# Optimization experiments

Hardware: AMD Instinct MI355X
Metric: run time of the kernel (lower is better)

Reference implementation:

```python
import jax, jax.numpy as jnp
import numpy as np

B, T, D_MODEL, N_HEADS = 2, 2048, 1024, 16
HEAD_DIM = D_MODEL // N_HEADS
EPS = 1e-6
ROPE_BASE = 10000.0


def _rope_cos_sin(seq_len, dim, offset=0, dtype=jnp.float32):
    half = dim // 2
    inv_freq = 1.0 / (ROPE_BASE ** (jnp.arange(half, dtype=jnp.float32) / half))
    pos = jnp.arange(offset, offset + seq_len, dtype=jnp.float32)
    freqs = pos[:, None] * inv_freq[None, :]              # (T, half)
    emb = jnp.concatenate([freqs, freqs], axis=-1)        # (T, dim)
    return jnp.cos(emb).astype(dtype), jnp.sin(emb).astype(dtype)


def _rotate_half(x):
    x1, x2 = jnp.split(x, 2, axis=-1)
    return jnp.concatenate([-x2, x1], axis=-1)


def setup_inputs() -> dict:
    key = jax.random.key(0)
    k1, k2, k3 = jax.random.split(key, 3)
    x = jax.random.normal(k1, (B, T, D_MODEL), dtype=jnp.float32)
    norm_w = jnp.ones((D_MODEL,), dtype=jnp.float32)
    w_qkv = jax.random.normal(k2, (3 * D_MODEL, D_MODEL), dtype=jnp.float32) * 0.02
    w_out = jax.random.normal(k3, (D_MODEL, D_MODEL), dtype=jnp.float32) * 0.02
    return {"x": x, "norm_w": norm_w, "w_qkv": w_qkv, "w_out": w_out}


def reference(x, norm_w, w_qkv, w_out):
    # RMSNorm (pre-norm)
    h = x * jax.lax.rsqrt(jnp.mean(jnp.square(x), axis=-1, keepdims=True) + EPS) * norm_w
    # Fused QKV projection: (B,T,3*D)
    qkv = jnp.einsum('btd,ed->bte', h, w_qkv).reshape(B, T, 3, N_HEADS, HEAD_DIM)
    q, k, v = qkv[:, :, 0], qkv[:, :, 1], qkv[:, :, 2]   # each (B,T,H,Dh)
    # RoPE on q, k (offset=0)
    cos, sin = _rope_cos_sin(T, HEAD_DIM, dtype=q.dtype)
    cos = cos[None, :, None, :]
    sin = sin[None, :, None, :]
    q = q * cos + _rotate_half(q) * sin
    k = k * cos + _rotate_half(k) * sin
    # Causal scaled dot-product attention
    scale = 1.0 / np.sqrt(HEAD_DIM)
    scores = jnp.einsum('bqhd,bkhd->bhqk', q, k) * scale  # (B,H,T,T)
    causal = jnp.tril(jnp.ones((T, T), dtype=bool))
    scores = jnp.where(causal[None, None], scores, jnp.finfo(scores.dtype).min)
    attn = jax.nn.softmax(scores, axis=-1)
    out = jnp.einsum('bhqk,bkhd->bqhd', attn, v).reshape(B, T, D_MODEL)
    out = jnp.einsum('btd,ed->bte', out, w_out)
    return x + out
```

## Files before the change

### kernel.cpp

```cpp
#include <hip/hip_runtime.h>
#include <math.h>

typedef unsigned short u16;
typedef unsigned int u32;
typedef __attribute__((ext_vector_type(4))) float f32x4;
typedef __attribute__((ext_vector_type(8))) short s16x8;

#define GLL16(g, l) __builtin_amdgcn_global_load_lds( \
    (const __attribute__((address_space(1))) void*)(g), \
    (__attribute__((address_space(3))) void*)(l), 16, 0, 0)

#define MFMA16(a, b, c) __builtin_amdgcn_mfma_f32_16x16x32_bf16(a, b, c, 0, 0, 0)

__device__ __forceinline__ u16 f2bf(float f) {
  union { float f; u32 u; } v; v.f = f;
  u32 r = v.u + 0x7FFFu + ((v.u >> 16) & 1u);
  return (u16)(r >> 16);
}
__device__ __forceinline__ float bf2f(u16 h) {
  union { u32 u; float f; } v; v.u = ((u32)h) << 16;
  return v.f;
}
__device__ __forceinline__ u32 pk2bf(float lo, float hi) {
  union { float f; u32 u; } a, b; a.f = lo; b.f = hi;
  return __builtin_amdgcn_perm(b.u + 0x8000u, a.u + 0x8000u, 0x07060302u);
}
__device__ __forceinline__ float fexp2(float x) {
#if __has_builtin(__builtin_amdgcn_exp2f)
  return __builtin_amdgcn_exp2f(x);
#else
  return exp2f(x);
#endif
}

__global__ __launch_bounds__(256) void prep_kernel(const float* __restrict__ x,
                                                   const float* __restrict__ wgt,
                                                   const float* __restrict__ w_qkv,
                                                   const float* __restrict__ w_out,
                                                   u16* __restrict__ h,
                                                   u16* __restrict__ wqkv_b,
                                                   u16* __restrict__ wout_b) {
  __shared__ float red[4];
  const int bid = blockIdx.x, tid = threadIdx.x;
  if (bid < 4096) {
    const int row = bid;
    const float4 v = *(const float4*)&x[(size_t)row * 1024 + tid * 4];
    float ss = v.x * v.x + v.y * v.y + v.z * v.z + v.w * v.w;
    ss += __shfl_xor(ss, 1);  ss += __shfl_xor(ss, 2);  ss += __shfl_xor(ss, 4);
    ss += __shfl_xor(ss, 8);  ss += __shfl_xor(ss, 16); ss += __shfl_xor(ss, 32);
    if ((tid & 63) == 0) red[tid >> 6] = ss;
    __syncthreads();
    const float tot = red[0] + red[1] + red[2] + red[3];
    const float s = rsqrtf(tot * (1.0f / 1024.0f) + 1e-6f);
    const float4 g = *(const float4*)&wgt[tid * 4];
    uint2 o;
    o.x = (u32)f2bf(v.x * s * g.x) | ((u32)f2bf(v.y * s * g.y) << 16);
    o.y = (u32)f2bf(v.z * s * g.z) | ((u32)f2bf(v.w * s * g.w) << 16);
    *(uint2*)&h[(size_t)row * 1024 + tid * 4] = o;
  } else if (bid < 7168) {
    int i = (bid - 4096) * 256 + tid;
    float4 v = ((const float4*)w_qkv)[i];
    uint2 o;
    o.x = (u32)f2bf(v.x) | ((u32)f2bf(v.y) << 16);
    o.y = (u32)f2bf(v.z) | ((u32)f2bf(v.w) << 16);
    ((uint2*)wqkv_b)[i] = o;
  } else {
    int i = (bid - 7168) * 256 + tid;
    float4 v = ((const float4*)w_out)[i];
    uint2 o;
    o.x = (u32)f2bf(v.x) | ((u32)f2bf(v.y) << 16);
    o.y = (u32)f2bf(v.z) | ((u32)f2bf(v.w) << 16);
    ((uint2*)wout_b)[i] = o;
  }
}

template <int EPI>
__global__ __launch_bounds__(256) void gemm_bt(const u16* __restrict__ A,
                                               const u16* __restrict__ Bt,
                                               u16* __restrict__ Cb,
                                               float* __restrict__ Cf,
                                               const float* __restrict__ resid,
                                               int M, int N, int K) {
  __shared__ __attribute__((aligned(16))) u16 As[128 * 32];
  __shared__ __attribute__((aligned(16))) u16 Bs[128 * 32];
  const int tid = threadIdx.x;
  const int w = tid >> 6, lane = tid & 63;
  const int quad = lane >> 4, l16 = lane & 15;
  const int gm0 = blockIdx.y * 128, gn0 = blockIdx.x * 128;
  const int wm = (w & 1) * 64, wn = (w >> 1) * 64;

  f32x4 acc[4][4] = {};

  for (int k0 = 0; k0 < K; k0 += 32) {
    __syncthreads();
    if (w < 2) {
      #pragma unroll
      for (int i = 0; i < 4; ++i) {
        int sb = (w * 4 + i) * 64;
        int slot = sb + lane;
        int m = slot >> 2, c = (slot & 3) ^ (m & 3);
        GLL16(A + (size_t)(gm0 + m) * K + k0 + c * 8, &As[sb * 8]);
      }
    } else {
      #pragma unroll
      for (int i = 0; i < 4; ++i) {
        int sb = ((w - 2) * 4 + i) * 64;
        int slot = sb + lane;
        int n = slot >> 2, c = (slot & 3) ^ (n & 3);
        GLL16(Bt + (size_t)(gn0 + n) * K + k0 + c * 8, &Bs[sb * 8]);
      }
    }
    __syncthreads();
    s16x8 aF[4], bF[4];
    #pragma unroll
    for (int i = 0; i < 4; ++i) {
      int m = wm + i * 16 + l16;
      aF[i] = *(const s16x8*)&As[(m * 4 + (quad ^ (m & 3))) * 8];
    }
    #pragma unroll
    for (int j = 0; j < 4; ++j) {
      int n = wn + j * 16 + l16;
      bF[j] = *(const s16x8*)&Bs[(n * 4 + (quad ^ (n & 3))) * 8];
    }
    #pragma unroll
    for (int i = 0; i < 4; ++i)
      #pragma unroll
      for (int j = 0; j < 4; ++j)
        acc[i][j] = MFMA16(aF[i], bF[j], acc[i][j]);
  }

  #pragma unroll
  for (int i = 0; i < 4; ++i) {
    int row0 = gm0 + wm + i * 16 + quad * 4;
    #pragma unroll
    for (int j = 0; j < 4; ++j) {
      int col = gn0 + wn + j * 16 + l16;
      #pragma unroll
      for (int r = 0; r < 4; ++r) {
        size_t idx = (size_t)(row0 + r) * N + col;
        if (EPI == 0) Cb[idx] = f2bf(acc[i][j][r]);
        else          Cf[idx] = acc[i][j][r] + resid[idx];
      }
    }
  }
}

__global__ __launch_bounds__(512, 2) void gemm256(const u16* __restrict__ A,
                                                  const u16* __restrict__ Bt,
                                                  u16* __restrict__ Cb) {
  __shared__ __attribute__((aligned(16))) char smem[131072];
  const int tid = threadIdx.x;
  const int w = tid >> 6, lane = tid & 63;
  const int quad = lane >> 4, l16 = lane & 15;
  const int wr = w >> 2, wc = w & 3;
  const int rsw = l16 & 7;
  const int id = blockIdx.x;
  const int sw = (id & 7) * 24 + (id >> 3);
  const int by = sw / 12, bx = sw - by * 12;
  const int gm0 = by * 256, gn0 = bx * 256;
  const int scg = (lane & 7) ^ (lane >> 3);

  auto STAGE_HALF = [&](int kt, int part) {
    const int sb = (kt & 1) * 65536 + (part >> 1) * 32768 + (part & 1) * 16384;
    const u16* src = (part >> 1) ? Bt : A;
    const int g0 = ((part >> 1) ? gn0 : gm0) + (part & 1) * 128;
    const int k0 = kt * 64;
    #pragma unroll
    for (int q = 0; q < 2; ++q) {
      int r = q * 64 + (tid >> 3);
      GLL16(src + (size_t)(g0 + r) * 1024 + k0 + scg * 8,
            smem + sb + q * 8192 + w * 1024);
    }
  };

  f32x4 acc[8][4] = {};

  #pragma unroll
  for (int n = 0; n < 8; ++n) STAGE_HALF(n >> 2, n & 3);
  __syncthreads();

  for (int kt = 0; kt < 16; ++kt) {
    const char* Ab = smem + (kt & 1) * 65536;
    const char* Bb = Ab + 32768;
    const int arow = wr * 128 + l16;
    const int brow = wc * 64 + l16;
    s16x8 aA[4][2], bB[4][2];

    #pragma unroll
    for (int fi = 0; fi < 4; ++fi) {
      const char* p = Ab + (arow + fi * 16) * 128;
      aA[fi][0] = *(const s16x8*)(p + ((quad ^ rsw) * 16));
      aA[fi][1] = *(const s16x8*)(p + (((4 + quad) ^ rsw) * 16));
    }
    #pragma unroll
    for (int fj = 0; fj < 2; ++fj) {
      const char* p = Bb + (brow + fj * 16) * 128;
      bB[fj][0] = *(const s16x8*)(p + ((quad ^ rsw) * 16));
      bB[fj][1] = *(const s16x8*)(p + (((4 + quad) ^ rsw) * 16));
    }
    if (kt >= 1 && kt < 15) STAGE_HALF(kt + 1, 0);
    __builtin_amdgcn_s_barrier();
    asm volatile("s_waitcnt lgkmcnt(0)" ::: "memory");
    __builtin_amdgcn_sched_barrier(0);
    __builtin_amdgcn_s_setprio(1);
    #pragma unroll
    for (int fi = 0; fi < 4; ++fi)
      #pragma unroll
      for (int fj = 0; fj < 2; ++fj) {
        acc[fi][fj] = MFMA16(aA[fi][0], bB[fj][0], acc[fi][fj]);
        acc[fi][fj] = MFMA16(aA[fi][1], bB[fj][1], acc[fi][fj]);
      }
    __builtin_amdgcn_s_setprio(0);
    __builtin_amdgcn_s_barrier();
    asm volatile("" ::: "memory");

    #pragma unroll
    for (int fj = 0; fj < 2; ++fj) {
      const char* p = Bb + (brow + (2 + fj) * 16) * 128;
      bB[2 + fj][0] = *(const s16x8*)(p + ((quad ^ rsw) * 16));
      bB[2 + fj][1] = *(const s16x8*)(p + (((4 + quad) ^ rsw) * 16));
    }
    if (kt >= 1 && kt < 15) STAGE_HALF(kt + 1, 1);
    __builtin_amdgcn_s_barrier();
    asm volatile("s_waitcnt lgkmcnt(0)" ::: "memory");
    __builtin_amdgcn_sched_barrier(0);
    __builtin_amdgcn_s_setprio(1);
    #pragma unroll
    for (int fi = 0; fi < 4; ++fi)
      #pragma unroll
      for (int fj = 0; fj < 2; ++fj) {
        acc[fi][2 + fj] = MFMA16(aA[fi][0], bB[2 + fj][0], acc[fi][2 + fj]);
        acc[fi][2 + fj] = MFMA16(aA[fi][1], bB[2 + fj][1], acc[fi][2 + fj]);
      }
    __builtin_amdgcn_s_setprio(0);
    __builtin_amdgcn_s_barrier();
    asm volatile("" ::: "memory");

    #pragma unroll
    for (int fi = 0; fi < 4; ++fi) {
      const char* p = Ab + (arow + (4 + fi) * 16) * 128;
      aA[fi][0] = *(const s16x8*)(p + ((quad ^ rsw) * 16));
      aA[fi][1] = *(const s16x8*)(p + (((4 + quad) ^ rsw) * 16));
    }
    if (kt < 14) STAGE_HALF(kt + 2, 2);
    __builtin_amdgcn_s_barrier();
    asm volatile("s_waitcnt lgkmcnt(0)" ::: "memory");
    __builtin_amdgcn_sched_barrier(0);
    __builtin_amdgcn_s_setprio(1);
    #pragma unroll
    for (int fi = 0; fi < 4; ++fi)
      #pragma unroll
      for (int fj = 0; fj < 2; ++fj) {
        acc[4 + fi][fj] = MFMA16(aA[fi][0], bB[fj][0], acc[4 + fi][fj]);
        acc[4 + fi][fj] = MFMA16(aA[fi][1], bB[fj][1], acc[4 + fi][fj]);
      }
    __builtin_amdgcn_s_setprio(0);
    __builtin_amdgcn_s_barrier();
    asm volatile("" ::: "memory");

    if (kt < 14) STAGE_HALF(kt + 2, 3);
    __builtin_amdgcn_s_barrier();
    __builtin_amdgcn_s_setprio(1);
    #pragma unroll
    for (int fi = 0; fi < 4; ++fi)
      #pragma unroll
      for (int fj = 0; fj < 2; ++fj) {
        acc[4 + fi][2 + fj] = MFMA16(aA[fi][0], bB[2 + fj][0], acc[4 + fi][2 + fj]);
        acc[4 + fi][2 + fj] = MFMA16(aA[fi][1], bB[2 + fj][1], acc[4 + fi][2 + fj]);
      }
    __builtin_amdgcn_s_setprio(0);
    if (kt < 14)      asm volatile("s_waitcnt vmcnt(4)" ::: "memory");
    else if (kt < 15) asm volatile("s_waitcnt vmcnt(0)" ::: "memory");
    __builtin_amdgcn_s_barrier();
    asm volatile("" ::: "memory");
  }

  #pragma unroll
  for (int g = 0; g < 8; ++g) {
    const int row0 = gm0 + wr * 128 + g * 16 + quad * 4;
    #pragma unroll
    for (int fj = 0; fj < 4; ++fj) {
      const int col = gn0 + wc * 64 + fj * 16 + l16;
      #pragma unroll
      for (int r = 0; r < 4; ++r)
        Cb[(size_t)(row0 + r) * 3072 + col] = f2bf(acc[g][fj][r]);
    }
  }
}

__global__ __launch_bounds__(256) void rope_kernel(const u16* __restrict__ qkv,
                                                   u16* __restrict__ Qr,
                                                   u16* __restrict__ Kr,
                                                   u16* __restrict__ Vt) {
  const int tt = blockIdx.x, bh = blockIdx.y;
  const int b = bh >> 4, h = bh & 15;
  const int tid = threadIdx.x;
  const float QSCALE = 0.125f * 1.4426950408889634f;

  #pragma unroll
  for (int ii = 0; ii < 8; ++ii) {
    int idx = ii * 256 + tid;
    int tl = idx >> 5, jj = idx & 31;
    int t = tt * 64 + tl;
    size_t mrow = (size_t)(b * 2048 + t) * 3072 + h * 64;
    float q1 = bf2f(qkv[mrow + jj]),        q2 = bf2f(qkv[mrow + 32 + jj]);
    float k1 = bf2f(qkv[mrow + 1024 + jj]), k2 = bf2f(qkv[mrow + 1024 + 32 + jj]);
    float invf = exp2f(-(float)jj * (13.287712379549449f / 32.0f));
    float ang = (float)t * invf;
    float sn, cs;
    sincosf(ang, &sn, &cs);
    size_t orow = (size_t)(bh * 2048 + t) * 64;
    Qr[orow + jj]      = f2bf((q1 * cs - q2 * sn) * QSCALE);
    Qr[orow + 32 + jj] = f2bf((q2 * cs + q1 * sn) * QSCALE);
    Kr[orow + jj]      = f2bf(k1 * cs - k2 * sn);
    Kr[orow + 32 + jj] = f2bf(k2 * cs + k1 * sn);
  }

  __shared__ __attribute__((aligned(16))) u16 Vl[64][72];
  for (int s = tid; s < 512; s += 256) {
    int r = s >> 3, c8 = (s & 7) * 8;
    *(uint4*)&Vl[r][c8] =
        *(const uint4*)&qkv[(size_t)(b * 2048 + tt * 64 + r) * 3072 + 2048 + h * 64 + c8];
  }
  __syncthreads();
  for (int s = tid; s < 512; s += 256) {
    int d = s >> 3, t8 = (s & 7) * 8;
    u16 tmp[8];
    #pragma unroll
    for (int k = 0; k < 8; ++k) tmp[k] = Vl[t8 + k][d];
    *(uint4*)&Vt[(size_t)(bh * 64 + d) * 2048 + tt * 64 + t8] = *(uint4*)tmp;
  }
}

__global__ __launch_bounds__(512, 2) void attn_kernel(const u16* __restrict__ Qr,
                                                      const u16* __restrict__ Kr,
                                                      const u16* __restrict__ Vt,
                                                      u16* __restrict__ AO) {
  __shared__ __attribute__((aligned(16))) char smem[102400];
  const int tid = threadIdx.x;
  const int w = tid >> 6, lane = tid & 63;
  const int wq = w & 3, wp = w >> 2;
  const int quad = lane >> 4, l16 = lane & 15;
  const int id = blockIdx.x;
  const int bh = id & 31;
  const int c  = id >> 5;
  const int b = bh >> 4, h = bh & 15;
  const size_t qkb = (size_t)bh * (2048 * 64);
  const size_t vtb = (size_t)bh * (64 * 2048);
  u16* Pw = (u16*)(smem + 65536 + w * 4608);

  const int srow = lane >> 3;
  const int scg  = (lane & 7) ^ srow;
  const int smat = w & 1, stp = (w >> 1) & 1, shalf = (w >> 2) & 1;

  auto STAGE = [&](int j0, int d) {
    const int jn = j0 + stp;
    if (smat == 0) {
      #pragma unroll
      for (int ii = 0; ii < 4; ++ii) {
        int i = shalf * 4 + ii;
        GLL16(Kr + qkb + (size_t)(jn * 64 + i * 8 + srow) * 64 + scg * 8,
              smem + (stp * 2 + d) * 8192 + i * 1024);
      }
    } else {
      #pragma unroll
      for (int ii = 0; ii < 4; ++ii) {
        int i = shalf * 4 + ii;
        GLL16(Vt + vtb + (size_t)(i * 8 + srow) * 2048 + jn * 64 + scg * 8,
              smem + 32768 + (stp * 2 + d) * 8192 + i * 1024);
      }
    }
  };

  for (int t = 0; t < 2; ++t) {
    const int qblk = t ? (15 - c) : c;
    const int q0w = qblk * 128 + wq * 32;
    const int steps = qblk + 1;

    s16x8 bQ[2][2];
    #pragma unroll
    for (int s = 0; s < 2; ++s)
      #pragma unroll
      for (int hf = 0; hf < 2; ++hf)
        bQ[s][hf] = *(const s16x8*)&Qr[qkb + (size_t)(q0w + s * 16 + l16) * 64 + hf * 32 + quad * 8];

    f32x4 O[2][4] = {};
    float l_run[2] = {0.0f, 0.0f};

    STAGE(0, 0);
    __syncthreads();

    for (int st = 0; st < steps; ++st) {
      const int cur = st & 1;
      if (st + 1 < steps) STAGE(2 * st + 2, cur ^ 1);

      const int j = 2 * st + wp;
      if (j * 64 <= q0w + 31) {
        const u16* Kb = (const u16*)(smem + (wp * 2 + cur) * 8192);
        const u16* Vb = (const u16*)(smem + 32768 + (wp * 2 + cur) * 8192);
        const bool masked = (j * 64 + 63 > q0w);
        const int rsw = (l16 & 7);

        s16x8 aK[4][2];
        #pragma unroll
        for (int kt = 0; kt < 4; ++kt)
          #pragma unroll
          for (int hf = 0; hf < 2; ++hf)
            aK[kt][hf] = *(const s16x8*)&Kb[(kt * 16 + l16) * 64 + (((hf * 4 + quad) ^ rsw) * 8)];

        f32x4 S[2][4];
        __builtin_amdgcn_s_setprio(1);
        #pragma unroll
        for (int kt = 0; kt < 4; ++kt)
          #pragma unroll
          for (int s = 0; s < 2; ++s) {
            f32x4 z = {};
            z = MFMA16(aK[kt][0], bQ[s][0], z);
            S[s][kt] = MFMA16(aK[kt][1], bQ[s][1], z);
          }
        __builtin_amdgcn_s_setprio(0);

        if (masked) {
          #pragma unroll
          for (int s = 0; s < 2; ++s) {
            int q = q0w + s * 16 + l16;
            #pragma unroll
            for (int kt = 0; kt < 4; ++kt) {
              int key0 = j * 64 + kt * 16 + quad * 4;
              #pragma unroll
              for (int r = 0; r < 4; ++r)
                if (key0 + r > q) S[s][kt][r] = -1e30f;
            }
          }
        }

        #pragma unroll
        for (int s = 0; s < 2; ++s) {
          float sum = 0.0f;
          #pragma unroll
          for (int kt = 0; kt < 4; ++kt) {
            #pragma unroll
            for (int r = 0; r < 4; ++r) {
              float e = fexp2(S[s][kt][r]);
              S[s][kt][r] = e;
              sum += e;
            }
          }
          sum += __shfl_xor(sum, 16);
          sum += __shfl_xor(sum, 32);
          l_run[s] += sum;
          #pragma unroll
          for (int kt = 0; kt < 4; ++kt) {
            uint2 pw;
            pw.x = pk2bf(S[s][kt][0], S[s][kt][1]);
            pw.y = pk2bf(S[s][kt][2], S[s][kt][3]);
            *(uint2*)&Pw[s * 1152 + l16 * 72 + kt * 16 + quad * 4] = pw;
          }
        }

        s16x8 bP[2][2];
        #pragma unroll
        for (int s = 0; s < 2; ++s) {
          bP[s][0] = *(const s16x8*)&Pw[s * 1152 + l16 * 72 + quad * 8];
          bP[s][1] = *(const s16x8*)&Pw[s * 1152 + l16 * 72 + 32 + quad * 8];
        }
        s16x8 aV[4][2];
        #pragma unroll
        for (int dt = 0; dt < 4; ++dt)
          #pragma unroll
          for (int hf = 0; hf < 2; ++hf)
            aV[dt][hf] = *(const s16x8*)&Vb[(dt * 16 + l16) * 64 + (((hf * 4 + quad) ^ rsw) * 8)];

        __builtin_amdgcn_s_setprio(1);
        #pragma unroll
        for (int dt = 0; dt < 4; ++dt)
          #pragma unroll
          for (int s = 0; s < 2; ++s) {
            O[s][dt] = MFMA16(aV[dt][0], bP[s][0], O[s][dt]);
            O[s][dt] = MFMA16(aV[dt][1], bP[s][1], O[s][dt]);
          }
        __builtin_amdgcn_s_setprio(0);
      }

      __syncthreads();
    }

    if (wp == 1) {
      float* Lsl = (float*)(smem + 65536 + wq * 512);
      Lsl[lane]      = l_run[0];
      Lsl[64 + lane] = l_run[1];
      f32x4* slot = (f32x4*)smem + wq * 512;
      #pragma unroll
      for (int s = 0; s < 2; ++s)
        #pragma unroll
        for (int dt = 0; dt < 4; ++dt)
          slot[(s * 4 + dt) * 64 + lane] = O[s][dt];
    }
    __syncthreads();
    if (wp == 0) {
      const float* Lsl = (const float*)(smem + 65536 + wq * 512);
      const f32x4* slot = (const f32x4*)smem + wq * 512;
      #pragma unroll
      for (int s = 0; s < 2; ++s) {
        float l_tot = l_run[s] + Lsl[s * 64 + lane];
        float inv = __builtin_amdgcn_rcpf(l_tot);
        int q = q0w + s * 16 + l16;
        #pragma unroll
        for (int dt = 0; dt < 4; ++dt) {
          f32x4 o = O[s][dt] + slot[(s * 4 + dt) * 64 + lane];
          uint2 ow;
          ow.x = pk2bf(o[0] * inv, o[1] * inv);
          ow.y = pk2bf(o[2] * inv, o[3] * inv);
          *(uint2*)&AO[(size_t)(b * 2048 + q) * 1024 + h * 64 + dt * 16 + quad * 4] = ow;
        }
      }
    }
    __syncthreads();
  }
}

extern "C" void kernel_launch(void* const* d_in, const int* in_sizes, int n_in,
                              void* d_out, int out_size, void* d_ws, size_t ws_size,
                              hipStream_t stream) {
  const float* x      = (const float*)d_in[0];
  const float* norm_w = (const float*)d_in[1];
  const float* w_qkv  = (const float*)d_in[2];
  const float* w_out  = (const float*)d_in[3];
  float* out = (float*)d_out;

  u16* ws     = (u16*)d_ws;
  u16* wqkv_b = ws;
  u16* wout_b = wqkv_b + 3145728;
  u16* h_b    = wout_b + 1048576;
  u16* qkv_b  = h_b + 4194304;
  u16* Qr     = qkv_b + 12582912;
  u16* Kr     = Qr + 4194304;
  u16* Vt     = Kr + 4194304;
  u16* AO     = Vt + 4194304;

  prep_kernel<<<8192, 256, 0, stream>>>(x, norm_w, w_qkv, w_out, h_b, wqkv_b, wout_b);
  gemm256<<<192, 512, 0, stream>>>(h_b, wqkv_b, qkv_b);
  rope_kernel<<<dim3(32, 32), 256, 0, stream>>>(qkv_b, Qr, Kr, Vt);
  attn_kernel<<<256, 512, 0, stream>>>(Qr, Kr, Vt, AO);
  gemm_bt<1><<<dim3(8, 32), 256, 0, stream>>>(AO, wout_b, nullptr, out, x,
                                              4096, 1024, 1024);
}
```

Measured before the change: 185.4 us.

## Collapse four-phase GEMM main loop into two phases with fewer barriers

Restructures the QKV GEMM inner loop from four barrier-separated MFMA sub-phases into two. All B fragments and the first half of A are loaded up front, the A tile for k+1 is staged early, and the B tile for k+2 is staged after a single barrier. The prologue now stages only the tiles needed under the new ordering, with a partial vmcnt wait. The aim is to cut barrier and waitcnt overhead per k-step and overlap global-to-LDS loads with larger MFMA blocks. The cost is more live fragment registers and less fine-grained interleaving of memory and MFMA work.

```diff
diff --git a/kernel.cpp b/kernel.cpp
--- a/kernel.cpp
+++ b/kernel.cpp
@@ -175,9 +175,11 @@
 
   f32x4 acc[8][4] = {};
 
-  #pragma unroll
-  for (int n = 0; n < 8; ++n) STAGE_HALF(n >> 2, n & 3);
-  __syncthreads();
+  STAGE_HALF(0, 0); STAGE_HALF(0, 1);
+  STAGE_HALF(0, 2); STAGE_HALF(0, 3);
+  STAGE_HALF(1, 2); STAGE_HALF(1, 3);
+  asm volatile("s_waitcnt vmcnt(4)" ::: "memory");
+  __builtin_amdgcn_s_barrier();
 
   for (int kt = 0; kt < 16; ++kt) {
     const char* Ab = smem + (kt & 1) * 65536;
@@ -193,48 +195,23 @@
       aA[fi][1] = *(const s16x8*)(p + (((4 + quad) ^ rsw) * 16));
     }
     #pragma unroll
-    for (int fj = 0; fj < 2; ++fj) {
+    for (int fj = 0; fj < 4; ++fj) {
       const char* p = Bb + (brow + fj * 16) * 128;
       bB[fj][0] = *(const s16x8*)(p + ((quad ^ rsw) * 16));
       bB[fj][1] = *(const s16x8*)(p + (((4 + quad) ^ rsw) * 16));
     }
-    if (kt >= 1 && kt < 15) STAGE_HALF(kt + 1, 0);
-    __builtin_amdgcn_s_barrier();
-    asm volatile("s_waitcnt lgkmcnt(0)" ::: "memory");
-    __builtin_amdgcn_sched_barrier(0);
+
+    if (kt < 15) { STAGE_HALF(kt + 1, 0); STAGE_HALF(kt + 1, 1); }
+
     __builtin_amdgcn_s_setprio(1);
     #pragma unroll
     for (int fi = 0; fi < 4; ++fi)
       #pragma unroll
-      for (int fj = 0; fj < 2; ++fj) {
+      for (int fj = 0; fj < 4; ++fj) {
         acc[fi][fj] = MFMA16(aA[fi][0], bB[fj][0], acc[fi][fj]);
         acc[fi][fj] = MFMA16(aA[fi][1], bB[fj][1], acc[fi][fj]);
       }
     __builtin_amdgcn_s_setprio(0);
-    __builtin_amdgcn_s_barrier();
-    asm volatile("" ::: "memory");
-
-    #pragma unroll
-    for (int fj = 0; fj < 2; ++fj) {
-      const char* p = Bb + (brow + (2 + fj) * 16) * 128;
-      bB[2 + fj][0] = *(const s16x8*)(p + ((quad ^ rsw) * 16));
-      bB[2 + fj][1] = *(const s16x8*)(p + (((4 + quad) ^ rsw) * 16));
-    }
-    if (kt >= 1 && kt < 15) STAGE_HALF(kt + 1, 1);
-    __builtin_amdgcn_s_barrier();
-    asm volatile("s_waitcnt lgkmcnt(0)" ::: "memory");
-    __builtin_amdgcn_sched_barrier(0);
-    __builtin_amdgcn_s_setprio(1);
-    #pragma unroll
-    for (int fi = 0; fi < 4; ++fi)
-      #pragma unroll
-      for (int fj = 0; fj < 2; ++fj) {
-        acc[fi][2 + fj] = MFMA16(aA[fi][0], bB[2 + fj][0], acc[fi][2 + fj]);
-        acc[fi][2 + fj] = MFMA16(aA[fi][1], bB[2 + fj][1], acc[fi][2 + fj]);
-      }
-    __builtin_amdgcn_s_setprio(0);
-    __builtin_amdgcn_s_barrier();
-    asm volatile("" ::: "memory");
 
     #pragma unroll
     for (int fi = 0; fi < 4; ++fi) {
@@ -242,37 +219,26 @@
       aA[fi][0] = *(const s16x8*)(p + ((quad ^ rsw) * 16));
       aA[fi][1] = *(const s16x8*)(p + (((4 + quad) ^ rsw) * 16));
     }
-    if (kt < 14) STAGE_HALF(kt + 2, 2);
-    __builtin_amdgcn_s_barrier();
-    asm volatile("s_waitcnt lgkmcnt(0)" ::: "memory");
-    __builtin_amdgcn_sched_barrier(0);
+
     __builtin_amdgcn_s_setprio(1);
     #pragma unroll
     for (int fi = 0; fi < 4; ++fi)
       #pragma unroll
-      for (int fj = 0; fj < 2; ++fj) {
+      for (int fj = 0; fj < 4; ++fj) {
         acc[4 + fi][fj] = MFMA16(aA[fi][0], bB[fj][0], acc[4 + fi][fj]);
         acc[4 + fi][fj] = MFMA16(aA[fi][1], bB[fj][1], acc[4 + fi][fj]);
       }
     __builtin_amdgcn_s_setprio(0);
+
     __builtin_amdgcn_s_barrier();
-    asm volatile("" ::: "memory");
-
-    if (kt < 14) STAGE_HALF(kt + 2, 3);
+
+    if (kt < 14) {
+      STAGE_HALF(kt + 2, 2); STAGE_HALF(kt + 2, 3);
+      asm volatile("s_waitcnt vmcnt(4)" ::: "memory");
+    } else if (kt == 14) {
+      asm volatile("s_waitcnt vmcnt(0)" ::: "memory");
+    }
     __builtin_amdgcn_s_barrier();
-    __builtin_amdgcn_s_setprio(1);
-    #pragma unroll
-    for (int fi = 0; fi < 4; ++fi)
-      #pragma unroll
-      for (int fj = 0; fj < 2; ++fj) {
-        acc[4 + fi][2 + fj] = MFMA16(aA[fi][0], bB[2 + fj][0], acc[4 + fi][2 + fj]);
-        acc[4 + fi][2 + fj] = MFMA16(aA[fi][1], bB[2 + fj][1], acc[4 + fi][2 + fj]);
-      }
-    __builtin_amdgcn_s_setprio(0);
-    if (kt < 14)      asm volatile("s_waitcnt vmcnt(4)" ::: "memory");
-    else if (kt < 15) asm volatile("s_waitcnt vmcnt(0)" ::: "memory");
-    __builtin_amdgcn_s_barrier();
-    asm volatile("" ::: "memory");
   }
 
   #pragma unroll
```

Result: no change. 183.9 us (-0.8%).
